# Kernel optimization log

Hardware: AMD Instinct MI355X
Metric: run time of the kernel (lower is better)

Reference implementation:

```python
import jax, jax.numpy as jnp
import numpy as np

V_THRESHOLD = 1.0
V_RESET = 0.0
TAU = 2.0
SURROGATE_PARAM = 0.5  # 'zo' (rectangular window) surrogate half-width


@jax.custom_vjp
def act_fun(x):
    # Heaviside step: spike if membrane exceeds threshold
    return (x > 0).astype(x.dtype)


def _act_fwd(x):
    return act_fun(x), x


def _act_bwd(x, g):
    # zero-order / rectangular surrogate gradient:
    # d spike / dx = 1/(2a) * 1[|x| < a]
    a = SURROGATE_PARAM
    grad = g * (jnp.abs(x) < a).astype(g.dtype) / (2.0 * a)
    return (grad,)


act_fun.defvjp(_act_fwd, _act_bwd)


def lif_forward(X):
    # X: [B, T, N] -> spikes [B, T, N]
    Xt = jnp.swapaxes(X, 0, 1)  # [T, B, N]

    def step(mem, x_t):
        # leaky integration toward (input + v_reset)
        mem = mem + (x_t + V_RESET - mem) / TAU
        spike = act_fun(mem - V_THRESHOLD)
        # hard reset to v_reset where spiked
        mem = (1.0 - spike) * mem + V_RESET * spike
        return mem, spike

    mem0 = jnp.zeros(Xt.shape[1:], dtype=X.dtype)
    _, spikes = jax.lax.scan(step, mem0, Xt)  # spikes: [T, B, N]
    return jnp.swapaxes(spikes, 0, 1)  # [B, T, N]


def setup_inputs() -> dict:
    key = jax.random.key(0)
    B, T, N = 128, 32, 8192
    X = jax.random.normal(key, (B, T, N), dtype=jnp.float32)
    return {"X": X}


def reference(X):
    return lif_forward(X)
```

## Files before the change

### kernel.cpp

```cpp
#include <hip/hip_runtime.h>


#define T_STEPS 32

__global__ __launch_bounds__(256) void lif_fwd_kernel(
    const float4* __restrict__ X, float4* __restrict__ out,
    int N4 , int TN4 )
{
    const int idx = blockIdx.x * blockDim.x + threadIdx.x;
    const int b = idx / N4;
    const int n = idx - b * N4;
    const size_t base = (size_t)b * (size_t)TN4 + (size_t)n;

    float m0 = 0.f, m1 = 0.f, m2 = 0.f, m3 = 0.f;

#pragma unroll
    for (int t = 0; t < T_STEPS; ++t) {
        const float4 x = X[base + (size_t)t * (size_t)N4];

        m0 = m0 + (x.x - m0) * 0.5f;
        m1 = m1 + (x.y - m1) * 0.5f;
        m2 = m2 + (x.z - m2) * 0.5f;
        m3 = m3 + (x.w - m3) * 0.5f;

        float4 s;
        s.x = (m0 - 1.0f > 0.0f) ? 1.0f : 0.0f;
        s.y = (m1 - 1.0f > 0.0f) ? 1.0f : 0.0f;
        s.z = (m2 - 1.0f > 0.0f) ? 1.0f : 0.0f;
        s.w = (m3 - 1.0f > 0.0f) ? 1.0f : 0.0f;

        m0 = (s.x != 0.0f) ? 0.0f : m0;
        m1 = (s.y != 0.0f) ? 0.0f : m1;
        m2 = (s.z != 0.0f) ? 0.0f : m2;
        m3 = (s.w != 0.0f) ? 0.0f : m3;

        out[base + (size_t)t * (size_t)N4] = s;
    }
}

extern "C" void kernel_launch(void* const* d_in, const int* in_sizes, int n_in,
                              void* d_out, int out_size, void* d_ws, size_t ws_size,
                              hipStream_t stream) {
    const float4* X = (const float4*)d_in[0];
    float4* out = (float4*)d_out;

    const int N = 8192;
    const int T = T_STEPS;
    const int total = in_sizes[0];
    const int B = total / (T * N);

    const int N4 = N / 4;
    const int TN4 = T * N4;
    const int threads = B * N4;

    const int block = 256;
    const int grid = (threads + block - 1) / block;

    lif_fwd_kernel<<<grid, block, 0, stream>>>(X, out, N4, TN4);
}
```

Measured before the change: 237.6 us.

## Process four float4 columns per thread with explicit batched asm loads

Each thread now owns four float4 column groups spaced 64 apart and walks time with four inline-asm global loads per step, waiting on all of them before computing. Grid and block are shrunk so the launch has a quarter as many threads, and sizes become compile-time constants. The aim is more independent loads per thread and less index arithmetic. The trade-off is far fewer resident waves and a full vmcnt wait every timestep with the time loop no longer unrolled, which can limit memory-level parallelism.

Result: no change. 234.7 us (-1.2%).

```diff
diff --git a/kernel.cpp b/kernel.cpp
--- a/kernel.cpp
+++ b/kernel.cpp
@@ -2,39 +2,64 @@
 
 
 #define T_STEPS 32
+#define N4 2048
+#define TN4 (T_STEPS * N4)
 
-__global__ __launch_bounds__(256) void lif_fwd_kernel(
-    const float4* __restrict__ X, float4* __restrict__ out,
-    int N4 , int TN4 )
+__device__ __forceinline__ float4 lif_step4(const float4 x, float* m) {
+    float4 s;
+    m[0] = m[0] + (x.x - m[0]) * 0.5f;
+    m[1] = m[1] + (x.y - m[1]) * 0.5f;
+    m[2] = m[2] + (x.z - m[2]) * 0.5f;
+    m[3] = m[3] + (x.w - m[3]) * 0.5f;
+    s.x = (m[0] - 1.0f > 0.0f) ? 1.0f : 0.0f;
+    s.y = (m[1] - 1.0f > 0.0f) ? 1.0f : 0.0f;
+    s.z = (m[2] - 1.0f > 0.0f) ? 1.0f : 0.0f;
+    s.w = (m[3] - 1.0f > 0.0f) ? 1.0f : 0.0f;
+    m[0] = (s.x != 0.0f) ? 0.0f : m[0];
+    m[1] = (s.y != 0.0f) ? 0.0f : m[1];
+    m[2] = (s.z != 0.0f) ? 0.0f : m[2];
+    m[3] = (s.w != 0.0f) ? 0.0f : m[3];
+    return s;
+}
+
+__global__ __launch_bounds__(128) void lif_fwd_kernel(
+    const float4* __restrict__ X, float4* __restrict__ out)
 {
-    const int idx = blockIdx.x * blockDim.x + threadIdx.x;
-    const int b = idx / N4;
-    const int n = idx - b * N4;
-    const size_t base = (size_t)b * (size_t)TN4 + (size_t)n;
+    const int b       = blockIdx.x >> 2;
+    const int quarter = blockIdx.x & 3;
+    const int wave    = threadIdx.x >> 6;
+    const int lane    = threadIdx.x & 63;
+    const int col0    = quarter * 512 + wave * 256 + lane;
+    const size_t base = (size_t)b * (size_t)TN4 + (size_t)col0;
 
-    float m0 = 0.f, m1 = 0.f, m2 = 0.f, m3 = 0.f;
+    const float4* p0 = X + base;
+    const float4* p1 = p0 + 64;
+    const float4* p2 = p0 + 128;
+    const float4* p3 = p0 + 192;
+    float4* q = out + base;
 
+    float m[16];
 #pragma unroll
+    for (int i = 0; i < 16; ++i) m[i] = 0.f;
+
     for (int t = 0; t < T_STEPS; ++t) {
-        const float4 x = X[base + (size_t)t * (size_t)N4];
+        float4 x0, x1, x2, x3;
+        asm volatile(
+            "global_load_dwordx4 %0, %4, off\n\t"
+            "global_load_dwordx4 %1, %5, off\n\t"
+            "global_load_dwordx4 %2, %6, off\n\t"
+            "global_load_dwordx4 %3, %7, off\n\t"
+            "s_waitcnt vmcnt(0)"
+            : "=&v"(x0), "=&v"(x1), "=&v"(x2), "=&v"(x3)
+            : "v"(p0), "v"(p1), "v"(p2), "v"(p3)
+            : "memory");
 
-        m0 = m0 + (x.x - m0) * 0.5f;
-        m1 = m1 + (x.y - m1) * 0.5f;
-        m2 = m2 + (x.z - m2) * 0.5f;
-        m3 = m3 + (x.w - m3) * 0.5f;
+        q[0]   = lif_step4(x0, m + 0);
+        q[64]  = lif_step4(x1, m + 4);
+        q[128] = lif_step4(x2, m + 8);
+        q[192] = lif_step4(x3, m + 12);
 
-        float4 s;
-        s.x = (m0 - 1.0f > 0.0f) ? 1.0f : 0.0f;
-        s.y = (m1 - 1.0f > 0.0f) ? 1.0f : 0.0f;
-        s.z = (m2 - 1.0f > 0.0f) ? 1.0f : 0.0f;
-        s.w = (m3 - 1.0f > 0.0f) ? 1.0f : 0.0f;
-
-        m0 = (s.x != 0.0f) ? 0.0f : m0;
-        m1 = (s.y != 0.0f) ? 0.0f : m1;
-        m2 = (s.z != 0.0f) ? 0.0f : m2;
-        m3 = (s.w != 0.0f) ? 0.0f : m3;
-
-        out[base + (size_t)t * (size_t)N4] = s;
+        p0 += N4; p1 += N4; p2 += N4; p3 += N4; q += N4;
     }
 }
 
@@ -44,17 +69,11 @@
     const float4* X = (const float4*)d_in[0];
     float4* out = (float4*)d_out;
 
-    const int N = 8192;
-    const int T = T_STEPS;
     const int total = in_sizes[0];
-    const int B = total / (T * N);
+    const int B = total / (T_STEPS * 8192);
 
-    const int N4 = N / 4;
-    const int TN4 = T * N4;
-    const int threads = B * N4;
+    const int block = 128;
+    const int grid = B * 4;
 
-    const int block = 256;
-    const int grid = (threads + block - 1) / block;
-
-    lif_fwd_kernel<<<grid, block, 0, stream>>>(X, out, N4, TN4);
+    lif_fwd_kernel<<<grid, block, 0, stream>>>(X, out);
 }
```
